# Performance work log

Hardware: AMD Instinct MI355X
Metric: run time of the kernel (lower is better)

## Reference

```python
import jax, jax.numpy as jnp
import numpy as np

# dims
R, K, N, V = 2, 3, 16384, 256          # r_len, num feat keys, nodes, raw feat dim
E, L, VE = 1, 8, 128                   # num extra keys, extra seq len, extra raw dim
LK, OUT = 1, 64                        # num label keys, out_feats (num classes)
IN, HID = 256, 512                     # in_feats, hidden
C = K + E + LK                         # num_channels for grouped conv / LayerNorm
LN_EPS = 1e-5


def _xav(key, shape, fan_in, fan_out):
    s = np.sqrt(2.0 / (fan_in + fan_out)).astype(np.float32)
    return jax.random.normal(key, shape, dtype=jnp.float32) * s


def setup_inputs() -> dict:
    key = jax.random.key(0)
    ks = jax.random.split(key, 16)
    inp = {}
    # forward args (dict-of-tensor structures flattened to stacked arrays in sorted-key order)
    inp["raw_feats"] = jax.random.normal(ks[0], (R, K, N, V), dtype=jnp.float32)
    inp["extra_feats"] = jax.random.normal(ks[1], (R, E, N, L, VE), dtype=jnp.float32)
    inp["label_feats"] = jax.random.normal(ks[2], (R, LK, N, OUT), dtype=jnp.float32)
    # per-relation embedding tables (original: uniform(-0.5,0.5); scaled for numeric tameness)
    inp["feat_emb"] = jax.random.uniform(ks[3], (R, K, V, IN), minval=-0.05, maxval=0.05, dtype=jnp.float32)
    inp["extra_emb"] = jax.random.uniform(ks[4], (R, E, VE, IN), minval=-0.05, maxval=0.05, dtype=jnp.float32)
    inp["label_emb"] = jax.random.uniform(ks[5], (R, LK, OUT, IN), minval=-0.05, maxval=0.05, dtype=jnp.float32)
    # sigmoid-attention weight vectors
    inp["w_extra"] = _xav(ks[6], (E, IN), IN, 1)      # embed_weight_r_extra
    inp["w_r"] = _xav(ks[7], (R, HID), HID, 1)        # embed_weight_r
    inp["w_global"] = _xav(ks[8], (HID,), HID, 1)     # self.w
    # grouped conv1x1 stack + LayerNorm([C,HID]) + PReLU (x2)
    inp["W1"] = _xav(ks[9], (C, IN, HID), IN, HID)
    inp["b1"] = jnp.zeros((C, HID), jnp.float32)
    inp["g1"] = jnp.ones((C, HID), jnp.float32)
    inp["be1"] = jnp.zeros((C, HID), jnp.float32)
    inp["a1"] = jnp.float32(0.25)
    inp["W2"] = _xav(ks[10], (C, HID, HID), HID, HID)
    inp["b2"] = jnp.zeros((C, HID), jnp.float32)
    inp["g2"] = jnp.ones((C, HID), jnp.float32)
    inp["be2"] = jnp.zeros((C, HID), jnp.float32)
    inp["a2"] = jnp.float32(0.25)
    # FeedForwardNet (n_layers_2 = 2)
    inp["Wf1"] = _xav(ks[11], (HID, HID), HID, HID)
    inp["bf1"] = jnp.zeros((HID,), jnp.float32)
    inp["af"] = jnp.float32(0.25)
    inp["Wf2"] = _xav(ks[12], (HID, OUT), HID, OUT)
    inp["bf2"] = jnp.zeros((OUT,), jnp.float32)
    return inp


def _prelu(x, a):
    return jnp.where(x >= 0, x, a * x)


def _ln(x, g, b):
    # LayerNorm over last two dims ([C, HID]) as in nn.LayerNorm([num_channels, hidden])
    m = jnp.mean(x, axis=(-2, -1), keepdims=True)
    v = jnp.var(x, axis=(-2, -1), keepdims=True)
    return (x - m) * jax.lax.rsqrt(v + LN_EPS) * g + b


def _attn_pool(f, w):
    # f: [N, C, D], w: [D] -> softmax(sigmoid(f @ w)) over C, weighted sum -> [N, D]
    gv = jax.nn.softmax(jax.nn.sigmoid(f @ w), axis=-1)
    return jnp.einsum('ncd,nc->nd', f, gv)


def reference(raw_feats, extra_feats, label_feats, feat_emb, extra_emb, label_emb,
              w_extra, w_r, w_global, W1, b1, g1, be1, a1, W2, b2, g2, be2, a2,
              Wf1, bf1, af, Wf2, bf2):
    outs = []
    for r in range(R):  # small fixed ensemble loop (structurally distinct params)
        mapped = jnp.einsum('knv,kvd->nkd', raw_feats[r], feat_emb[r])        # [N,K,IN]
        me = jnp.einsum('enlv,evd->enld', extra_feats[r], extra_emb[r])       # [E,N,L,IN]
        extra_out = jax.vmap(_attn_pool)(me, w_extra)                          # [E,N,IN]
        ml = jnp.einsum('knc,kcd->nkd', label_feats[r], label_emb[r])         # [N,LK,IN]
        feats = jnp.concatenate([mapped, jnp.moveaxis(extra_out, 0, 1), ml], axis=1)  # [N,C,IN]
        x = jnp.einsum('ncm,cmh->nch', feats, W1) + b1                         # grouped conv1x1
        x = _prelu(_ln(x, g1, be1), a1)
        x = jnp.einsum('nch,chk->nck', x, W2) + b2
        x = _prelu(_ln(x, g2, be2), a2)
        outs.append(_attn_pool(x, w_r[r]))                                     # [N,HID]
    h = jnp.stack(outs, axis=1)                                                # [N,R,HID]
    final = _attn_pool(h, w_global)                                            # [N,HID]
    y = _prelu(final @ Wf1 + bf1, af)
    return y @ Wf2 + bf2
```

## Files before the change

kernel.cpp:

```cpp
#include <hip/hip_runtime.h>


typedef unsigned short bf16_t;
using ushort8v = __attribute__((ext_vector_type(8))) unsigned short;
using bf16x8   = __attribute__((ext_vector_type(8))) __bf16;
using f32x4    = __attribute__((ext_vector_type(4))) float;

__device__ __forceinline__ float bf2f(bf16_t u) {
    return __uint_as_float(((unsigned int)u) << 16);
}
__device__ __forceinline__ bf16_t f2bf(float f) {
    unsigned int u = __float_as_uint(f);
    u += 0x7FFFu + ((u >> 16) & 1u);
    return (bf16_t)(u >> 16);
}
__device__ __forceinline__ float ld1(const void* p, long i, int dt) {
    return dt ? bf2f(((const bf16_t*)p)[i]) : ((const float*)p)[i];
}
__device__ __forceinline__ float4 ld4(const void* p, long i, int dt) {
    if (dt) {
        ushort4 v = *(const ushort4*)((const bf16_t*)p + i);
        return make_float4(bf2f(v.x), bf2f(v.y), bf2f(v.z), bf2f(v.w));
    }
    return *(const float4*)((const float*)p + i);
}
__device__ __forceinline__ ushort8v ld8bf(const void* p, long i, int dt) {
    if (dt) return *(const ushort8v*)((const bf16_t*)p + i);
    const float* f = (const float*)p + i;
    float4 a = *(const float4*)f, b = *(const float4*)(f + 4);
    ushort8v r;
    r[0] = f2bf(a.x); r[1] = f2bf(a.y); r[2] = f2bf(a.z); r[3] = f2bf(a.w);
    r[4] = f2bf(b.x); r[5] = f2bf(b.y); r[6] = f2bf(b.z); r[7] = f2bf(b.w);
    return r;
}
__device__ __forceinline__ float decode_scalar(const void* p, int isbf) {
    if (!isbf) return *(const float*)p;
    unsigned int u = *(const unsigned int*)p;
    if ((u & 0xFFFFu) == 0u) return __uint_as_float(u);
    return bf2f((bf16_t)(u & 0xFFFFu));
}
__device__ __forceinline__ float wave_reduce(float v) {
#pragma unroll
    for (int o = 32; o > 0; o >>= 1) v += __shfl_down(v, o, 64);
    return v;
}

__global__ void detect_k(const unsigned int* __restrict__ w, long nwords,
                         int* __restrict__ flag)
{
    const int lane = threadIdx.x;
    long idx = (long)lane * 997 + 13;
    if (idx >= nwords) idx = lane % (nwords > 0 ? nwords : 1);
    unsigned int word = w[idx];
    int e = (word >> 7) & 0xFF;
    int vote = (e >= 110 && e <= 134) ? 1 : 0;
    unsigned long long m = __ballot(vote);
    if (lane == 0) *flag = (__popcll(m) >= 32) ? 1 : 0;
}

__global__ __launch_bounds__(256) void transT_k(
    const void* __restrict__ in, long inoff, long sInZ, int Kd, int Nd,
    bf16_t* __restrict__ out, long outoff, long sOutZ,
    const int* __restrict__ flag)
{
    const int isbf = *flag;
    const long z = blockIdx.z;
    long idx = (long)blockIdx.x * 256 + threadIdx.x;
    if (idx >= (long)Kd * Nd) return;
    int k = (int)(idx / Nd), n = (int)(idx % Nd);
    out[outoff + z * sOutZ + (long)n * Kd + k] =
        f2bf(ld1(in, inoff + z * sInZ + idx, isbf));
}

__global__ __launch_bounds__(256) void fold_gemmT_k(
    const void* __restrict__ A, long aoff, long sAz, int lda,
    const void* __restrict__ B, long boff, long sBz, int ldb,
    bf16_t* __restrict__ CT, long coff, long sCz, int ldcT,
    int K, const int* __restrict__ flag)
{
    const int isbf = *flag;
    __shared__ __align__(16) float As[16][68];
    __shared__ __align__(16) float Bs[16][68];
    const int z = blockIdx.z, t = threadIdx.x;
    const int tx = t & 15, ty = t >> 4;
    const int am = t >> 2, ak = (t & 3) << 2;
    const int bn = tx << 2;
    const long aBase = aoff + z * sAz + (long)(blockIdx.y * 64 + am) * lda + ak;
    const long bBase = boff + z * sBz + (long)ty * ldb + blockIdx.x * 64 + bn;
    float acc[4][4] = {};
    for (int k0 = 0; k0 < K; k0 += 16) {
        float4 av = ld4(A, aBase + k0, isbf);
        float4 bv = ld4(B, bBase + (long)k0 * ldb, isbf);
        __syncthreads();
        As[ak + 0][am] = av.x; As[ak + 1][am] = av.y;
        As[ak + 2][am] = av.z; As[ak + 3][am] = av.w;
        *(float4*)&Bs[ty][bn] = bv;
        __syncthreads();
#pragma unroll
        for (int k = 0; k < 16; k++) {
            float4 a4 = *(const float4*)&As[k][ty << 2];
            float4 b4 = *(const float4*)&Bs[k][tx << 2];
            float ar[4] = {a4.x, a4.y, a4.z, a4.w};
            float br[4] = {b4.x, b4.y, b4.z, b4.w};
#pragma unroll
            for (int i = 0; i < 4; i++)
#pragma unroll
                for (int j = 0; j < 4; j++) acc[i][j] += ar[i] * br[j];
        }
    }
    const int cm = blockIdx.y * 64 + (ty << 2);
    const int cn = blockIdx.x * 64 + (tx << 2);
#pragma unroll
    for (int i = 0; i < 4; i++)
#pragma unroll
        for (int j = 0; j < 4; j++)
            CT[coff + z * sCz + (long)(cn + j) * ldcT + (cm + i)] = f2bf(acc[i][j]);
}

template <int BN_, int WNW_, int MODE, int CD>
__global__ __launch_bounds__(256) void mgemm(
    const void* __restrict__ A, int adt, long aoff, long sA1, long sA2, int lda,
    const bf16_t* __restrict__ BT, long boff, long sB1, long sB2,
    void* __restrict__ C, long coff, long sC1, long sC2, int ldc,
    const void* __restrict__ bias, long biasoff, long sBi1, long sBi2,
    const void* __restrict__ alpha_ptr, int K, int zdiv,
    const int* __restrict__ flag)
{
    constexpr int NJ = WNW_ / 16;
    const int isbf = *flag;
    const int adt_ = (adt == 2) ? isbf : adt;
    const int cdt = (CD == 2) ? isbf : 1;

    __shared__ __align__(16) unsigned short As[128 * 40];
    __shared__ __align__(16) unsigned short Bs[BN_ * 40];

    const int t = threadIdx.x;
    const int lane = t & 63, w = t >> 6;
    const int quad = lane >> 4, r16 = lane & 15;
    const int wy = w >> 1, wx = w & 1;
    const int z = blockIdx.z;
    const int zq = z / zdiv, zr = z % zdiv;
    const long blockM = (long)blockIdx.y * 128;
    const int  blockN = blockIdx.x * BN_;

    f32x4 acc[4][NJ];
    const f32x4 zero4 = {0.f, 0.f, 0.f, 0.f};
#pragma unroll
    for (int i = 0; i < 4; i++)
#pragma unroll
        for (int j = 0; j < NJ; j++) acc[i][j] = zero4;

    const long aBase = aoff + zq * sA1 + zr * sA2;
    const long bBase = boff + zq * sB1 + zr * sB2;

    for (int k0 = 0; k0 < K; k0 += 32) {
        ushort8v av[2], bv[BN_ / 64];
#pragma unroll
        for (int c = 0; c < 2; c++) {
            int lin = t + c * 256;
            int m = lin >> 2, kq = (lin & 3) * 8;
            av[c] = ld8bf(A, aBase + (blockM + m) * (long)lda + k0 + kq, adt_);
        }
#pragma unroll
        for (int c = 0; c < BN_ / 64; c++) {
            int lin = t + c * 256;
            int n = lin >> 2, kq = (lin & 3) * 8;
            bv[c] = *(const ushort8v*)(BT + bBase + (long)(blockN + n) * K + k0 + kq);
        }
        __syncthreads();
#pragma unroll
        for (int c = 0; c < 2; c++) {
            int lin = t + c * 256;
            int m = lin >> 2, kq = (lin & 3) * 8;
            *(ushort8v*)&As[m * 40 + kq] = av[c];
        }
#pragma unroll
        for (int c = 0; c < BN_ / 64; c++) {
            int lin = t + c * 256;
            int n = lin >> 2, kq = (lin & 3) * 8;
            *(ushort8v*)&Bs[n * 40 + kq] = bv[c];
        }
        __syncthreads();

        bf16x8 af[4], bfr[NJ];
#pragma unroll
        for (int i = 0; i < 4; i++) {
            int m = wy * 64 + i * 16 + r16;
            af[i] = __builtin_bit_cast(bf16x8, *(const ushort8v*)&As[m * 40 + quad * 8]);
        }
#pragma unroll
        for (int j = 0; j < NJ; j++) {
            int n = wx * WNW_ + j * 16 + r16;
            bfr[j] = __builtin_bit_cast(bf16x8, *(const ushort8v*)&Bs[n * 40 + quad * 8]);
        }
#pragma unroll
        for (int i = 0; i < 4; i++)
#pragma unroll
            for (int j = 0; j < NJ; j++)
                acc[i][j] = __builtin_amdgcn_mfma_f32_16x16x32_bf16(
                    af[i], bfr[j], acc[i][j], 0, 0, 0);
    }

    const float alpha = (MODE == 2) ? decode_scalar(alpha_ptr, isbf) : 0.f;
    const long cBase = coff + zq * sC1 + zr * sC2;
#pragma unroll
    for (int j = 0; j < NJ; j++) {
        const int n = blockN + wx * WNW_ + j * 16 + r16;
        const float bz = (MODE >= 1)
            ? ld1(bias, biasoff + zq * sBi1 + zr * sBi2 + n, isbf) : 0.f;
#pragma unroll
        for (int i = 0; i < 4; i++) {
            const long m0 = blockM + wy * 64 + i * 16 + quad * 4;
#pragma unroll
            for (int rg = 0; rg < 4; rg++) {
                float v = acc[i][j][rg] + bz;
                if (MODE == 2) v = (v >= 0.f) ? v : alpha * v;
                const long off = cBase + (m0 + rg) * (long)ldc + n;
                if (cdt) ((bf16_t*)C)[off] = f2bf(v);
                else     ((float*)C)[off] = v;
            }
        }
    }
}

__global__ __launch_bounds__(256) void pool_extra_k(
    const bf16_t* __restrict__ ME, long sMEz, const void* __restrict__ wx,
    float* __restrict__ EO, long sEOz, const int* __restrict__ flag)
{
    const int isbf = *flag;
    const int n = blockIdx.x, t = threadIdx.x;
    const bf16_t* base = ME + blockIdx.y * sMEz + (long)n * 2048;
    float v[8];
#pragma unroll
    for (int l = 0; l < 8; l++) v[l] = bf2f(base[l * 256 + t]);
    const float w = ld1(wx, t, isbf);
    __shared__ float red[8][4];
    const int lane = t & 63, wid = t >> 6;
#pragma unroll
    for (int l = 0; l < 8; l++) {
        float pr = wave_reduce(v[l] * w);
        if (lane == 0) red[l][wid] = pr;
    }
    __syncthreads();
    float gv[8], ssum = 0.f;
#pragma unroll
    for (int l = 0; l < 8; l++) {
        float sc = red[l][0] + red[l][1] + red[l][2] + red[l][3];
        float sg = 1.f / (1.f + expf(-sc));
        float e = expf(sg);
        gv[l] = e; ssum += e;
    }
    const float inv = 1.f / ssum;
    float o = 0.f;
#pragma unroll
    for (int l = 0; l < 8; l++) o += gv[l] * inv * v[l];
    EO[blockIdx.y * sEOz + (long)n * 256 + t] = o;
}

__global__ __launch_bounds__(256) void ln1_k(
    bf16_t* __restrict__ X, const void* __restrict__ g,
    const void* __restrict__ be, const void* __restrict__ alpha_ptr,
    const int* __restrict__ flag)
{
    const int isbf = *flag;
    const int n = blockIdx.x, t = threadIdx.x;
    bf16_t* row = X + (long)n * 2560;
    float v[10], s = 0.f, sq = 0.f;
#pragma unroll
    for (int i = 0; i < 10; i++) {
        float x = bf2f(row[i * 256 + t]);
        v[i] = x; s += x; sq += x * x;
    }
    __shared__ float redS[4], redQ[4];
    const int lane = t & 63, wid = t >> 6;
    float ws_ = wave_reduce(s), wq = wave_reduce(sq);
    if (lane == 0) { redS[wid] = ws_; redQ[wid] = wq; }
    __syncthreads();
    const float S = redS[0] + redS[1] + redS[2] + redS[3];
    const float Q = redQ[0] + redQ[1] + redQ[2] + redQ[3];
    const float mean = S * (1.f / 2560.f);
    const float rstd = rsqrtf(fmaxf(Q * (1.f / 2560.f) - mean * mean, 0.f) + 1e-5f);
    const float alpha = decode_scalar(alpha_ptr, isbf);
#pragma unroll
    for (int i = 0; i < 10; i++) {
        int e = i * 256 + t;
        float y = (v[i] - mean) * rstd * ld1(g, e, isbf) + ld1(be, e, isbf);
        row[e] = f2bf((y >= 0.f) ? y : alpha * y);
    }
}

__global__ __launch_bounds__(256) void ln2_pool_k(
    const bf16_t* __restrict__ X, long sXz, const void* __restrict__ g,
    const void* __restrict__ be, const void* __restrict__ alpha_ptr,
    const void* __restrict__ wr,
    bf16_t* __restrict__ H, const int* __restrict__ flag)
{
    const int isbf = *flag;
    const int n = blockIdx.x, t = threadIdx.x, rr = blockIdx.y;
    const bf16_t* row = X + rr * sXz + (long)n * 2560;
    float v[5][2], s = 0.f, sq = 0.f;
#pragma unroll
    for (int c = 0; c < 5; c++)
#pragma unroll
        for (int hi = 0; hi < 2; hi++) {
            float x = bf2f(row[c * 512 + hi * 256 + t]);
            v[c][hi] = x; s += x; sq += x * x;
        }
    __shared__ float redS[4], redQ[4];
    const int lane = t & 63, wid = t >> 6;
    float ws_ = wave_reduce(s), wq = wave_reduce(sq);
    if (lane == 0) { redS[wid] = ws_; redQ[wid] = wq; }
    __syncthreads();
    const float S = redS[0] + redS[1] + redS[2] + redS[3];
    const float Q = redQ[0] + redQ[1] + redQ[2] + redQ[3];
    const float mean = S * (1.f / 2560.f);
    const float rstd = rsqrtf(fmaxf(Q * (1.f / 2560.f) - mean * mean, 0.f) + 1e-5f);
    const float alpha = decode_scalar(alpha_ptr, isbf);
    const float w0 = ld1(wr, (long)rr * 512 + t, isbf);
    const float w1 = ld1(wr, (long)rr * 512 + t + 256, isbf);
    float p[5];
#pragma unroll
    for (int c = 0; c < 5; c++) {
        p[c] = 0.f;
#pragma unroll
        for (int hi = 0; hi < 2; hi++) {
            int e = c * 512 + hi * 256 + t;
            float y = (v[c][hi] - mean) * rstd * ld1(g, e, isbf) + ld1(be, e, isbf);
            y = (y >= 0.f) ? y : alpha * y;
            v[c][hi] = y;
            p[c] += y * (hi ? w1 : w0);
        }
    }
    __shared__ float redP[5][4];
#pragma unroll
    for (int c = 0; c < 5; c++) {
        float pr = wave_reduce(p[c]);
        if (lane == 0) redP[c][wid] = pr;
    }
    __syncthreads();
    float gv[5], ssum = 0.f;
#pragma unroll
    for (int c = 0; c < 5; c++) {
        float sc = redP[c][0] + redP[c][1] + redP[c][2] + redP[c][3];
        float sg = 1.f / (1.f + expf(-sc));
        float e = expf(sg);
        gv[c] = e; ssum += e;
    }
    const float inv = 1.f / ssum;
#pragma unroll
    for (int hi = 0; hi < 2; hi++) {
        float o = 0.f;
#pragma unroll
        for (int c = 0; c < 5; c++) o += gv[c] * inv * v[c][hi];
        H[(long)n * 1024 + rr * 512 + hi * 256 + t] = f2bf(o);
    }
}

__global__ __launch_bounds__(256) void gpool_k(
    const bf16_t* __restrict__ H, const void* __restrict__ wg,
    bf16_t* __restrict__ F, const int* __restrict__ flag)
{
    const int isbf = *flag;
    const int n = blockIdx.x, t = threadIdx.x;
    const bf16_t* base = H + (long)n * 1024;
    const float w0 = ld1(wg, t, isbf), w1 = ld1(wg, t + 256, isbf);
    float v[2][2], p[2];
#pragma unroll
    for (int r = 0; r < 2; r++) {
        v[r][0] = bf2f(base[r * 512 + t]);
        v[r][1] = bf2f(base[r * 512 + 256 + t]);
        p[r] = v[r][0] * w0 + v[r][1] * w1;
    }
    __shared__ float red[2][4];
    const int lane = t & 63, wid = t >> 6;
#pragma unroll
    for (int r = 0; r < 2; r++) {
        float pr = wave_reduce(p[r]);
        if (lane == 0) red[r][wid] = pr;
    }
    __syncthreads();
    float gv[2], ssum = 0.f;
#pragma unroll
    for (int r = 0; r < 2; r++) {
        float sc = red[r][0] + red[r][1] + red[r][2] + red[r][3];
        float sg = 1.f / (1.f + expf(-sc));
        float e = expf(sg);
        gv[r] = e; ssum += e;
    }
    const float inv = 1.f / ssum;
#pragma unroll
    for (int hi = 0; hi < 2; hi++) {
        F[(long)n * 512 + hi * 256 + t] =
            f2bf((gv[0] * v[0][hi] + gv[1] * v[1][hi]) * inv);
    }
}

extern "C" void kernel_launch(void* const* d_in, const int* in_sizes, int n_in,
                              void* d_out, int out_size, void* d_ws, size_t ws_size,
                              hipStream_t stream)
{
    const void* raw   = d_in[0];
    const void* extra = d_in[1];
    const void* lbl   = d_in[2];
    const void* femb  = d_in[3];
    const void* eemb  = d_in[4];
    const void* lemb  = d_in[5];
    const void* wx    = d_in[6];
    const void* wr    = d_in[7];
    const void* wg    = d_in[8];
    const void* W1    = d_in[9];
    const void* b1    = d_in[10];
    const void* g1    = d_in[11];
    const void* be1   = d_in[12];
    const void* a1    = d_in[13];
    const void* W2    = d_in[14];
    const void* b2    = d_in[15];
    const void* g2    = d_in[16];
    const void* be2   = d_in[17];
    const void* a2    = d_in[18];
    const void* Wf1   = d_in[19];
    const void* bf1   = d_in[20];
    const void* af    = d_in[21];
    const void* Wf2   = d_in[22];
    const void* bf2b  = d_in[23];

    int*    flag  = (int*)d_ws;
    bf16_t* MfT   = (bf16_t*)((char*)d_ws + 256);
    bf16_t* MlT   = MfT + 786432;
    bf16_t* W1c3T = MlT + 65536;
    bf16_t* W2T   = W1c3T + 131072;
    bf16_t* Wf1T  = W2T + 1310720;
    bf16_t* Wf2T  = Wf1T + 262144;
    bf16_t* eT    = Wf2T + 32768;
    char*   arena = (char*)(eT + 65536);
    const size_t fixedBytes = 256 + 2654208 * 2;

    int Nc = 16384;
    while (Nc > 128 && fixedBytes + (size_t)Nc * 24576 > ws_size) Nc >>= 1;
    const int NCH = 16384 / Nc;

    bf16_t* x1  = (bf16_t*)arena;
    bf16_t* x2  = (bf16_t*)(arena + (size_t)Nc * 10240);
    float*  eo  = (float*) (arena + (size_t)Nc * 20480);
    bf16_t* hbc = (bf16_t*)(arena + (size_t)Nc * 22528);
    bf16_t* mec = x1;
    bf16_t* fin = x2;
    bf16_t* zb  = x2 + (size_t)Nc * 512;

    dim3 blk(256);

    detect_k<<<1, 64, 0, stream>>>((const unsigned int*)raw,
                                   (long)in_sizes[0] / 2, flag);

    transT_k<<<dim3(1024, 1, 5), blk, 0, stream>>>(W2, 0, 262144, 512, 512,
                                                   W2T, 0, 262144, flag);
    transT_k<<<dim3(512, 1, 1), blk, 0, stream>>>(W1, 3L * 131072, 0, 256, 512,
                                                  W1c3T, 0, 0, flag);
    transT_k<<<dim3(1024, 1, 1), blk, 0, stream>>>(Wf1, 0, 0, 512, 512,
                                                   Wf1T, 0, 0, flag);
    transT_k<<<dim3(128, 1, 1), blk, 0, stream>>>(Wf2, 0, 0, 512, 64,
                                                  Wf2T, 0, 0, flag);
    transT_k<<<dim3(128, 1, 2), blk, 0, stream>>>(eemb, 0, 32768, 128, 256,
                                                  eT, 0, 32768, flag);

    for (int r = 0; r < 2; r++) {
        fold_gemmT_k<<<dim3(8, 4, 3), blk, 0, stream>>>(
            femb, (long)r * 196608, 65536, 256,
            W1, 0, 131072, 512,
            MfT, (long)r * 393216, 131072, 256, 256, flag);
    }
    fold_gemmT_k<<<dim3(8, 1, 2), blk, 0, stream>>>(
        lemb, 0, 16384, 256,
        W1, 4L * 131072, 0, 512,
        MlT, 0, 32768, 64, 256, flag);

    for (int c = 0; c < NCH; c++) {
        const long n0 = (long)c * Nc;

        mgemm<128, 64, 0, 1><<<dim3(2, Nc * 8 / 128, 2), blk, 0, stream>>>(
            extra, 2, n0 * 1024, 16777216, 0, 128,
            eT, 0, 32768, 0,
            mec, 0, (long)Nc * 8 * 256, 0, 256,
            nullptr, 0, 0, 0, nullptr, 128, 1, flag);
        pool_extra_k<<<dim3(Nc, 2), blk, 0, stream>>>(
            mec, (long)Nc * 8 * 256, wx, eo, (long)Nc * 256, flag);

        mgemm<128, 64, 1, 1><<<dim3(4, Nc / 128, 6), blk, 0, stream>>>(
            raw, 2, n0 * 256, 12582912, 4194304, 256,
            MfT, 0, 393216, 131072,
            x1, 0, (long)Nc * 2560, 512, 2560,
            b1, 0, 0, 512, nullptr, 256, 3, flag);
        mgemm<128, 64, 1, 1><<<dim3(4, Nc / 128, 2), blk, 0, stream>>>(
            eo, 0, 0, (long)Nc * 256, 0, 256,
            W1c3T, 0, 0, 0,
            x1, 3L * 512, (long)Nc * 2560, 0, 2560,
            b1, 3L * 512, 0, 0, nullptr, 256, 1, flag);
        mgemm<128, 64, 1, 1><<<dim3(4, Nc / 128, 2), blk, 0, stream>>>(
            lbl, 2, n0 * 64, 1048576, 0, 64,
            MlT, 0, 32768, 0,
            x1, 4L * 512, (long)Nc * 2560, 0, 2560,
            b1, 4L * 512, 0, 0, nullptr, 64, 1, flag);

        ln1_k<<<2 * Nc, blk, 0, stream>>>(x1, g1, be1, a1, flag);

        mgemm<128, 64, 1, 1><<<dim3(4, Nc / 128, 10), blk, 0, stream>>>(
            x1, 1, 0, (long)Nc * 2560, 512, 2560,
            W2T, 0, 0, 262144,
            x2, 0, (long)Nc * 2560, 512, 2560,
            b2, 0, 0, 512, nullptr, 512, 5, flag);

        ln2_pool_k<<<dim3(Nc, 2), blk, 0, stream>>>(
            x2, (long)Nc * 2560, g2, be2, a2, wr, hbc, flag);

        gpool_k<<<Nc, blk, 0, stream>>>(hbc, wg, fin, flag);

        mgemm<128, 64, 2, 1><<<dim3(4, Nc / 128, 1), blk, 0, stream>>>(
            fin, 1, 0, 0, 0, 512,
            Wf1T, 0, 0, 0,
            zb, 0, 0, 0, 512,
            bf1, 0, 0, 0, af, 512, 1, flag);
        mgemm<64, 32, 1, 2><<<dim3(1, Nc / 128, 1), blk, 0, stream>>>(
            zb, 1, 0, 0, 0, 512,
            Wf2T, 0, 0, 0,
            d_out, n0 * 64, 0, 0, 64,
            bf2b, 0, 0, 0, nullptr, 512, 1, flag);
    }
}
```

Measured before the change: 1.064 ms.

## Use direct global-to-LDS loads in GEMM and fuse pooling and LayerNorm kernels

The GEMM staging path now uses global_load_lds to copy bf16 tiles straight into unpadded LDS, replacing the register round-trip. The extra-feature GEMM and its sigmoid attention pool are fused into one kernel that writes a bf16 pooled output, so the 8x intermediate never goes to memory. LN2, the per-relation pool and the global pool are merged into one kernel that accumulates into LDS with shared atomics, and LN1 switches to 320-thread blocks with 8-wide vector loads. Dropping the LDS padding may add bank conflicts on the fragment reads, and the LDS atomics and bf16 rounding of the extra output change numerics slightly.

Result: slower. 1.355 ms (+27.4%).

```diff
diff --git a/kernel.cpp b/kernel.cpp
--- a/kernel.cpp
+++ b/kernel.cpp
@@ -1,4 +1,5 @@
 #include <hip/hip_runtime.h>
+#include <stdint.h>
 
 
 typedef unsigned short bf16_t;
@@ -43,6 +44,12 @@
 #pragma unroll
     for (int o = 32; o > 0; o >>= 1) v += __shfl_down(v, o, 64);
     return v;
+}
+__device__ __forceinline__ void gl2lds16(const void* g, void* l) {
+    using gptr_t = const __attribute__((address_space(1))) unsigned int*;
+    using lptr_t = __attribute__((address_space(3))) unsigned int*;
+    __builtin_amdgcn_global_load_lds((gptr_t)(uintptr_t)g, (lptr_t)(uintptr_t)l,
+                                     16, 0, 0);
 }
 
 __global__ void detect_k(const unsigned int* __restrict__ w, long nwords,
@@ -131,13 +138,15 @@
     const int adt_ = (adt == 2) ? isbf : adt;
     const int cdt = (CD == 2) ? isbf : 1;
 
-    __shared__ __align__(16) unsigned short As[128 * 40];
-    __shared__ __align__(16) unsigned short Bs[BN_ * 40];
+    __shared__ __align__(16) bf16_t As[128 * 32];
+    __shared__ __align__(16) bf16_t Bs[BN_ * 32];
 
     const int t = threadIdx.x;
-    const int lane = t & 63, w = t >> 6;
+    const int lane = t & 63, wv = t >> 6;
     const int quad = lane >> 4, r16 = lane & 15;
-    const int wy = w >> 1, wx = w & 1;
+    const int wy = wv >> 1, wxx = wv & 1;
+    const int srow = lane >> 2;
+    const int scol = (lane & 3) * 8;
     const int z = blockIdx.z;
     const int zq = z / zdiv, zr = z % zdiv;
     const long blockM = (long)blockIdx.y * 128;
@@ -154,45 +163,42 @@
     const long bBase = boff + zq * sB1 + zr * sB2;
 
     for (int k0 = 0; k0 < K; k0 += 32) {
-        ushort8v av[2], bv[BN_ / 64];
-#pragma unroll
-        for (int c = 0; c < 2; c++) {
-            int lin = t + c * 256;
-            int m = lin >> 2, kq = (lin & 3) * 8;
-            av[c] = ld8bf(A, aBase + (blockM + m) * (long)lda + k0 + kq, adt_);
-        }
-#pragma unroll
-        for (int c = 0; c < BN_ / 64; c++) {
-            int lin = t + c * 256;
-            int n = lin >> 2, kq = (lin & 3) * 8;
-            bv[c] = *(const ushort8v*)(BT + bBase + (long)(blockN + n) * K + k0 + kq);
-        }
-        __syncthreads();
-#pragma unroll
-        for (int c = 0; c < 2; c++) {
-            int lin = t + c * 256;
-            int m = lin >> 2, kq = (lin & 3) * 8;
-            *(ushort8v*)&As[m * 40 + kq] = av[c];
-        }
-#pragma unroll
-        for (int c = 0; c < BN_ / 64; c++) {
-            int lin = t + c * 256;
-            int n = lin >> 2, kq = (lin & 3) * 8;
-            *(ushort8v*)&Bs[n * 40 + kq] = bv[c];
+        __syncthreads();
+        if (adt_) {
+#pragma unroll
+            for (int s = 0; s < 2; s++) {
+                int rbase = wv * 32 + s * 16;
+                const bf16_t* g = (const bf16_t*)A + aBase
+                    + (blockM + rbase + srow) * (long)lda + k0 + scol;
+                gl2lds16(g, &As[rbase * 32]);
+            }
+        } else {
+#pragma unroll
+            for (int c = 0; c < 2; c++) {
+                int lin = t + c * 256;
+                int m = lin >> 2, kq = (lin & 3) * 8;
+                ushort8v v = ld8bf(A, aBase + (blockM + m) * (long)lda + k0 + kq, 0);
+                *(ushort8v*)&As[m * 32 + kq] = v;
+            }
+        }
+#pragma unroll
+        for (int s = 0; s < BN_ / 64; s++) {
+            int rbase = wv * (BN_ / 4) + s * 16;
+            const bf16_t* g = BT + bBase
+                + (long)(blockN + rbase + srow) * K + k0 + scol;
+            gl2lds16(g, &Bs[rbase * 32]);
         }
         __syncthreads();
 
         bf16x8 af[4], bfr[NJ];
 #pragma unroll
-        for (int i = 0; i < 4; i++) {
-            int m = wy * 64 + i * 16 + r16;
-            af[i] = __builtin_bit_cast(bf16x8, *(const ushort8v*)&As[m * 40 + quad * 8]);
-        }
-#pragma unroll
-        for (int j = 0; j < NJ; j++) {
-            int n = wx * WNW_ + j * 16 + r16;
-            bfr[j] = __builtin_bit_cast(bf16x8, *(const ushort8v*)&Bs[n * 40 + quad * 8]);
-        }
+        for (int i = 0; i < 4; i++)
+            af[i] = __builtin_bit_cast(bf16x8,
+                *(const ushort8v*)&As[(wy * 64 + i * 16 + r16) * 32 + quad * 8]);
+#pragma unroll
+        for (int j = 0; j < NJ; j++)
+            bfr[j] = __builtin_bit_cast(bf16x8,
+                *(const ushort8v*)&Bs[(wxx * WNW_ + j * 16 + r16) * 32 + quad * 8]);
 #pragma unroll
         for (int i = 0; i < 4; i++)
 #pragma unroll
@@ -205,7 +211,7 @@
     const long cBase = coff + zq * sC1 + zr * sC2;
 #pragma unroll
     for (int j = 0; j < NJ; j++) {
-        const int n = blockN + wx * WNW_ + j * 16 + r16;
+        const int n = blockN + wxx * WNW_ + j * 16 + r16;
         const float bz = (MODE >= 1)
             ? ld1(bias, biasoff + zq * sBi1 + zr * sBi2 + n, isbf) : 0.f;
 #pragma unroll
@@ -223,41 +229,151 @@
     }
 }
 
-__global__ __launch_bounds__(256) void pool_extra_k(
-    const bf16_t* __restrict__ ME, long sMEz, const void* __restrict__ wx,
-    float* __restrict__ EO, long sEOz, const int* __restrict__ flag)
+__global__ __launch_bounds__(256) void megemm_pool(
+    const void* __restrict__ A, long aoff, long sAr,
+    const bf16_t* __restrict__ BT, long sBr,
+    const void* __restrict__ wx,
+    bf16_t* __restrict__ EO, long sEOr,
+    const int* __restrict__ flag)
 {
     const int isbf = *flag;
-    const int n = blockIdx.x, t = threadIdx.x;
-    const bf16_t* base = ME + blockIdx.y * sMEz + (long)n * 2048;
-    float v[8];
-#pragma unroll
-    for (int l = 0; l < 8; l++) v[l] = bf2f(base[l * 256 + t]);
-    const float w = ld1(wx, t, isbf);
-    __shared__ float red[8][4];
-    const int lane = t & 63, wid = t >> 6;
-#pragma unroll
-    for (int l = 0; l < 8; l++) {
-        float pr = wave_reduce(v[l] * w);
-        if (lane == 0) red[l][wid] = pr;
+    __shared__ __align__(16) bf16_t As[128 * 32];
+    __shared__ __align__(16) bf16_t Bs[256 * 32];
+    __shared__ float sred[128][2];
+    __shared__ float gvs[128];
+
+    const int t = threadIdx.x;
+    const int lane = t & 63, wv = t >> 6;
+    const int quad = lane >> 4, r16 = lane & 15;
+    const int wy = wv >> 1, wxx = wv & 1;
+    const int srow = lane >> 2, scol = (lane & 3) * 8;
+    const int r = blockIdx.z;
+    const long blockM = (long)blockIdx.y * 128;
+
+    f32x4 acc[4][8];
+    const f32x4 zero4 = {0.f, 0.f, 0.f, 0.f};
+#pragma unroll
+    for (int i = 0; i < 4; i++)
+#pragma unroll
+        for (int j = 0; j < 8; j++) acc[i][j] = zero4;
+
+    const long aBase = aoff + (long)r * sAr;
+    const long bBase = (long)r * sBr;
+
+    for (int k0 = 0; k0 < 128; k0 += 32) {
+        __syncthreads();
+        if (isbf) {
+#pragma unroll
+            for (int s = 0; s < 2; s++) {
+                int rbase = wv * 32 + s * 16;
+                const bf16_t* g = (const bf16_t*)A + aBase
+                    + (blockM + rbase + srow) * 128L + k0 + scol;
+                gl2lds16(g, &As[rbase * 32]);
+            }
+        } else {
+#pragma unroll
+            for (int c = 0; c < 2; c++) {
+                int lin = t + c * 256;
+                int m = lin >> 2, kq = (lin & 3) * 8;
+                ushort8v v = ld8bf(A, aBase + (blockM + m) * 128L + k0 + kq, 0);
+                *(ushort8v*)&As[m * 32 + kq] = v;
+            }
+        }
+#pragma unroll
+        for (int s = 0; s < 4; s++) {
+            int rbase = wv * 64 + s * 16;
+            const bf16_t* g = BT + bBase + (long)(rbase + srow) * 128 + k0 + scol;
+            gl2lds16(g, &Bs[rbase * 32]);
+        }
+        __syncthreads();
+
+        bf16x8 af[4], bfr[8];
+#pragma unroll
+        for (int i = 0; i < 4; i++)
+            af[i] = __builtin_bit_cast(bf16x8,
+                *(const ushort8v*)&As[(wy * 64 + i * 16 + r16) * 32 + quad * 8]);
+#pragma unroll
+        for (int j = 0; j < 8; j++)
+            bfr[j] = __builtin_bit_cast(bf16x8,
+                *(const ushort8v*)&Bs[(wxx * 128 + j * 16 + r16) * 32 + quad * 8]);
+#pragma unroll
+        for (int i = 0; i < 4; i++)
+#pragma unroll
+            for (int j = 0; j < 8; j++)
+                acc[i][j] = __builtin_amdgcn_mfma_f32_16x16x32_bf16(
+                    af[i], bfr[j], acc[i][j], 0, 0, 0);
+    }
+
+    float wxv[8];
+#pragma unroll
+    for (int j = 0; j < 8; j++)
+        wxv[j] = ld1(wx, wxx * 128 + j * 16 + r16, isbf);
+
+    float pp[4][4];
+#pragma unroll
+    for (int i = 0; i < 4; i++)
+#pragma unroll
+        for (int rg = 0; rg < 4; rg++) {
+            float s = 0.f;
+#pragma unroll
+            for (int j = 0; j < 8; j++) s += acc[i][j][rg] * wxv[j];
+            pp[i][rg] = s;
+        }
+#pragma unroll
+    for (int o = 1; o < 16; o <<= 1)
+#pragma unroll
+        for (int i = 0; i < 4; i++)
+#pragma unroll
+            for (int rg = 0; rg < 4; rg++)
+                pp[i][rg] += __shfl_xor(pp[i][rg], o, 64);
+    if (r16 == 0) {
+#pragma unroll
+        for (int i = 0; i < 4; i++)
+#pragma unroll
+            for (int rg = 0; rg < 4; rg++)
+                sred[wy * 64 + i * 16 + quad * 4 + rg][wxx] = pp[i][rg];
     }
     __syncthreads();
-    float gv[8], ssum = 0.f;
-#pragma unroll
-    for (int l = 0; l < 8; l++) {
-        float sc = red[l][0] + red[l][1] + red[l][2] + red[l][3];
-        float sg = 1.f / (1.f + expf(-sc));
-        float e = expf(sg);
-        gv[l] = e; ssum += e;
-    }
-    const float inv = 1.f / ssum;
-    float o = 0.f;
-#pragma unroll
-    for (int l = 0; l < 8; l++) o += gv[l] * inv * v[l];
-    EO[blockIdx.y * sEOz + (long)n * 256 + t] = o;
-}
-
-__global__ __launch_bounds__(256) void ln1_k(
+    if (t < 16) {
+        float e[8], sm = 0.f;
+#pragma unroll
+        for (int l = 0; l < 8; l++) {
+            float sc = sred[t * 8 + l][0] + sred[t * 8 + l][1];
+            float sg = 1.f / (1.f + expf(-sc));
+            e[l] = expf(sg); sm += e[l];
+        }
+        float inv = 1.f / sm;
+#pragma unroll
+        for (int l = 0; l < 8; l++) gvs[t * 8 + l] = e[l] * inv;
+    }
+    __syncthreads();
+
+    float gvl[4][4];
+#pragma unroll
+    for (int i = 0; i < 4; i++)
+#pragma unroll
+        for (int rg = 0; rg < 4; rg++)
+            gvl[i][rg] = gvs[wy * 64 + i * 16 + quad * 4 + rg];
+
+#pragma unroll
+    for (int i = 0; i < 4; i++) {
+        const long nodeBase = (blockM + wy * 64 + i * 16) >> 3;
+        const int myNode = (int)nodeBase + (quad >> 1);
+#pragma unroll
+        for (int j = 0; j < 8; j++) {
+            float s = 0.f;
+#pragma unroll
+            for (int rg = 0; rg < 4; rg++) s += acc[i][j][rg] * gvl[i][rg];
+            s += __shfl_xor(s, 16, 64);
+            if ((quad & 1) == 0) {
+                int col = wxx * 128 + j * 16 + r16;
+                EO[(long)r * sEOr + (long)myNode * 256 + col] = f2bf(s);
+            }
+        }
+    }
+}
+
+__global__ __launch_bounds__(320) void ln1_k(
     bf16_t* __restrict__ X, const void* __restrict__ g,
     const void* __restrict__ be, const void* __restrict__ alpha_ptr,
     const int* __restrict__ flag)
@@ -265,134 +381,116 @@
     const int isbf = *flag;
     const int n = blockIdx.x, t = threadIdx.x;
     bf16_t* row = X + (long)n * 2560;
-    float v[10], s = 0.f, sq = 0.f;
-#pragma unroll
-    for (int i = 0; i < 10; i++) {
-        float x = bf2f(row[i * 256 + t]);
-        v[i] = x; s += x; sq += x * x;
-    }
-    __shared__ float redS[4], redQ[4];
+    const int e0 = t * 8;
+    ushort8v xv = *(const ushort8v*)&row[e0];
+    float v[8], s = 0.f, sq = 0.f;
+#pragma unroll
+    for (int k = 0; k < 8; k++) {
+        float x = bf2f(xv[k]);
+        v[k] = x; s += x; sq += x * x;
+    }
+    __shared__ float redS[5], redQ[5];
     const int lane = t & 63, wid = t >> 6;
     float ws_ = wave_reduce(s), wq = wave_reduce(sq);
     if (lane == 0) { redS[wid] = ws_; redQ[wid] = wq; }
     __syncthreads();
-    const float S = redS[0] + redS[1] + redS[2] + redS[3];
-    const float Q = redQ[0] + redQ[1] + redQ[2] + redQ[3];
+    float S = 0.f, Q = 0.f;
+#pragma unroll
+    for (int i = 0; i < 5; i++) { S += redS[i]; Q += redQ[i]; }
     const float mean = S * (1.f / 2560.f);
     const float rstd = rsqrtf(fmaxf(Q * (1.f / 2560.f) - mean * mean, 0.f) + 1e-5f);
     const float alpha = decode_scalar(alpha_ptr, isbf);
-#pragma unroll
-    for (int i = 0; i < 10; i++) {
-        int e = i * 256 + t;
-        float y = (v[i] - mean) * rstd * ld1(g, e, isbf) + ld1(be, e, isbf);
-        row[e] = f2bf((y >= 0.f) ? y : alpha * y);
-    }
-}
-
-__global__ __launch_bounds__(256) void ln2_pool_k(
-    const bf16_t* __restrict__ X, long sXz, const void* __restrict__ g,
+    ushort8v gv8 = ld8bf(g, e0, isbf), bv8 = ld8bf(be, e0, isbf);
+    ushort8v ov;
+#pragma unroll
+    for (int k = 0; k < 8; k++) {
+        float y = (v[k] - mean) * rstd * bf2f(gv8[k]) + bf2f(bv8[k]);
+        ov[k] = f2bf((y >= 0.f) ? y : alpha * y);
+    }
+    *(ushort8v*)&row[e0] = ov;
+}
+
+__global__ __launch_bounds__(320) void ln2_gpool_k(
+    const bf16_t* __restrict__ X, long sXr, const void* __restrict__ g,
     const void* __restrict__ be, const void* __restrict__ alpha_ptr,
-    const void* __restrict__ wr,
-    bf16_t* __restrict__ H, const int* __restrict__ flag)
-{
-    const int isbf = *flag;
-    const int n = blockIdx.x, t = threadIdx.x, rr = blockIdx.y;
-    const bf16_t* row = X + rr * sXz + (long)n * 2560;
-    float v[5][2], s = 0.f, sq = 0.f;
-#pragma unroll
-    for (int c = 0; c < 5; c++)
-#pragma unroll
-        for (int hi = 0; hi < 2; hi++) {
-            float x = bf2f(row[c * 512 + hi * 256 + t]);
-            v[c][hi] = x; s += x; sq += x * x;
-        }
-    __shared__ float redS[4], redQ[4];
-    const int lane = t & 63, wid = t >> 6;
-    float ws_ = wave_reduce(s), wq = wave_reduce(sq);
-    if (lane == 0) { redS[wid] = ws_; redQ[wid] = wq; }
-    __syncthreads();
-    const float S = redS[0] + redS[1] + redS[2] + redS[3];
-    const float Q = redQ[0] + redQ[1] + redQ[2] + redQ[3];
-    const float mean = S * (1.f / 2560.f);
-    const float rstd = rsqrtf(fmaxf(Q * (1.f / 2560.f) - mean * mean, 0.f) + 1e-5f);
-    const float alpha = decode_scalar(alpha_ptr, isbf);
-    const float w0 = ld1(wr, (long)rr * 512 + t, isbf);
-    const float w1 = ld1(wr, (long)rr * 512 + t + 256, isbf);
-    float p[5];
-#pragma unroll
-    for (int c = 0; c < 5; c++) {
-        p[c] = 0.f;
-#pragma unroll
-        for (int hi = 0; hi < 2; hi++) {
-            int e = c * 512 + hi * 256 + t;
-            float y = (v[c][hi] - mean) * rstd * ld1(g, e, isbf) + ld1(be, e, isbf);
-            y = (y >= 0.f) ? y : alpha * y;
-            v[c][hi] = y;
-            p[c] += y * (hi ? w1 : w0);
-        }
-    }
-    __shared__ float redP[5][4];
-#pragma unroll
-    for (int c = 0; c < 5; c++) {
-        float pr = wave_reduce(p[c]);
-        if (lane == 0) redP[c][wid] = pr;
-    }
-    __syncthreads();
-    float gv[5], ssum = 0.f;
-#pragma unroll
-    for (int c = 0; c < 5; c++) {
-        float sc = redP[c][0] + redP[c][1] + redP[c][2] + redP[c][3];
-        float sg = 1.f / (1.f + expf(-sc));
-        float e = expf(sg);
-        gv[c] = e; ssum += e;
-    }
-    const float inv = 1.f / ssum;
-#pragma unroll
-    for (int hi = 0; hi < 2; hi++) {
-        float o = 0.f;
-#pragma unroll
-        for (int c = 0; c < 5; c++) o += gv[c] * inv * v[c][hi];
-        H[(long)n * 1024 + rr * 512 + hi * 256 + t] = f2bf(o);
-    }
-}
-
-__global__ __launch_bounds__(256) void gpool_k(
-    const bf16_t* __restrict__ H, const void* __restrict__ wg,
+    const void* __restrict__ wr, const void* __restrict__ wg,
     bf16_t* __restrict__ F, const int* __restrict__ flag)
 {
     const int isbf = *flag;
     const int n = blockIdx.x, t = threadIdx.x;
-    const bf16_t* base = H + (long)n * 1024;
-    const float w0 = ld1(wg, t, isbf), w1 = ld1(wg, t + 256, isbf);
-    float v[2][2], p[2];
-#pragma unroll
+    const int lane = t & 63, wid = t >> 6;
+    const int e0 = t * 8;
+
+    __shared__ float hacc[2][512];
+    __shared__ float redS[2][5], redQ[2][5], redP[2][5], redG[2][5];
+    for (int i = t; i < 1024; i += 320) ((float*)hacc)[i] = 0.f;
+
+    const float alpha = decode_scalar(alpha_ptr, isbf);
+    ushort8v gv8 = ld8bf(g, e0, isbf), bv8 = ld8bf(be, e0, isbf);
+
     for (int r = 0; r < 2; r++) {
-        v[r][0] = bf2f(base[r * 512 + t]);
-        v[r][1] = bf2f(base[r * 512 + 256 + t]);
-        p[r] = v[r][0] * w0 + v[r][1] * w1;
-    }
-    __shared__ float red[2][4];
-    const int lane = t & 63, wid = t >> 6;
+        const bf16_t* row = X + (long)r * sXr + (long)n * 2560;
+        ushort8v xv = *(const ushort8v*)&row[e0];
+        float v[8], s = 0.f, sq = 0.f;
+#pragma unroll
+        for (int k = 0; k < 8; k++) {
+            float x = bf2f(xv[k]);
+            v[k] = x; s += x; sq += x * x;
+        }
+        float ws_ = wave_reduce(s), wq = wave_reduce(sq);
+        if (lane == 0) { redS[r][wid] = ws_; redQ[r][wid] = wq; }
+        __syncthreads();
+        float S = 0.f, Q = 0.f;
+#pragma unroll
+        for (int i = 0; i < 5; i++) { S += redS[r][i]; Q += redQ[r][i]; }
+        const float mean = S * (1.f / 2560.f);
+        const float rstd = rsqrtf(fmaxf(Q * (1.f / 2560.f) - mean * mean, 0.f) + 1e-5f);
+        float pc = 0.f;
+#pragma unroll
+        for (int k = 0; k < 8; k++) {
+            float y = (v[k] - mean) * rstd * bf2f(gv8[k]) + bf2f(bv8[k]);
+            y = (y >= 0.f) ? y : alpha * y;
+            v[k] = y;
+            pc += y * ld1(wr, (long)r * 512 + ((e0 + k) & 511), isbf);
+        }
+        float wp = wave_reduce(pc);
+        if (lane == 0) redP[r][wid] = wp;
+        __syncthreads();
+        float ssum = 0.f, eown = 0.f;
+#pragma unroll
+        for (int c = 0; c < 5; c++) {
+            float sg = 1.f / (1.f + expf(-redP[r][c]));
+            float e = expf(sg);
+            if (c == wid) eown = e;
+            ssum += e;
+        }
+        const float gvc = eown / ssum;
+#pragma unroll
+        for (int k = 0; k < 8; k++)
+            atomicAdd(&hacc[r][(e0 + k) & 511], v[k] * gvc);
+        __syncthreads();
+    }
+
+    float pr[2] = {0.f, 0.f};
+    for (int h = t; h < 512; h += 320) {
+        float w = ld1(wg, h, isbf);
+        pr[0] += hacc[0][h] * w;
+        pr[1] += hacc[1][h] * w;
+    }
 #pragma unroll
     for (int r = 0; r < 2; r++) {
-        float pr = wave_reduce(p[r]);
-        if (lane == 0) red[r][wid] = pr;
+        float wp = wave_reduce(pr[r]);
+        if (lane == 0) redG[r][wid] = wp;
     }
     __syncthreads();
-    float gv[2], ssum = 0.f;
-#pragma unroll
-    for (int r = 0; r < 2; r++) {
-        float sc = red[r][0] + red[r][1] + red[r][2] + red[r][3];
-        float sg = 1.f / (1.f + expf(-sc));
-        float e = expf(sg);
-        gv[r] = e; ssum += e;
-    }
-    const float inv = 1.f / ssum;
-#pragma unroll
-    for (int hi = 0; hi < 2; hi++) {
-        F[(long)n * 512 + hi * 256 + t] =
-            f2bf((gv[0] * v[0][hi] + gv[1] * v[1][hi]) * inv);
-    }
+    float sc0 = 0.f, sc1 = 0.f;
+#pragma unroll
+    for (int i = 0; i < 5; i++) { sc0 += redG[0][i]; sc1 += redG[1][i]; }
+    float eg0 = expf(1.f / (1.f + expf(-sc0)));
+    float eg1 = expf(1.f / (1.f + expf(-sc1)));
+    float inv = 1.f / (eg0 + eg1);
+    for (int h = t; h < 512; h += 320)
+        F[(long)n * 512 + h] = f2bf((eg0 * hacc[0][h] + eg1 * hacc[1][h]) * inv);
 }
 
 extern "C" void kernel_launch(void* const* d_in, const int* in_sizes, int n_in,
@@ -436,18 +534,16 @@
     const size_t fixedBytes = 256 + 2654208 * 2;
 
     int Nc = 16384;
-    while (Nc > 128 && fixedBytes + (size_t)Nc * 24576 > ws_size) Nc >>= 1;
+    while (Nc > 128 && fixedBytes + (size_t)Nc * 21504 > ws_size) Nc >>= 1;
     const int NCH = 16384 / Nc;
 
-    bf16_t* x1  = (bf16_t*)arena;
-    bf16_t* x2  = (bf16_t*)(arena + (size_t)Nc * 10240);
-    float*  eo  = (float*) (arena + (size_t)Nc * 20480);
-    bf16_t* hbc = (bf16_t*)(arena + (size_t)Nc * 22528);
-    bf16_t* mec = x1;
-    bf16_t* fin = x2;
-    bf16_t* zb  = x2 + (size_t)Nc * 512;
-
-    dim3 blk(256);
+    bf16_t* x1 = (bf16_t*)arena;
+    bf16_t* x2 = (bf16_t*)(arena + (size_t)Nc * 10240);
+    bf16_t* eo = (bf16_t*)(arena + (size_t)Nc * 20480);
+    bf16_t* fin = x1;
+    bf16_t* zb  = x1 + (size_t)Nc * 512;
+
+    dim3 blk(256), blk5(320);
 
     detect_k<<<1, 64, 0, stream>>>((const unsigned int*)raw,
                                    (long)in_sizes[0] / 2, flag);
@@ -477,13 +573,9 @@
     for (int c = 0; c < NCH; c++) {
         const long n0 = (long)c * Nc;
 
-        mgemm<128, 64, 0, 1><<<dim3(2, Nc * 8 / 128, 2), blk, 0, stream>>>(
-            extra, 2, n0 * 1024, 16777216, 0, 128,
-            eT, 0, 32768, 0,
-            mec, 0, (long)Nc * 8 * 256, 0, 256,
-            nullptr, 0, 0, 0, nullptr, 128, 1, flag);
-        pool_extra_k<<<dim3(Nc, 2), blk, 0, stream>>>(
-            mec, (long)Nc * 8 * 256, wx, eo, (long)Nc * 256, flag);
+        megemm_pool<<<dim3(1, Nc / 16, 2), blk, 0, stream>>>(
+            extra, n0 * 1024, 16777216,
+            eT, 32768, wx, eo, (long)Nc * 256, flag);
 
         mgemm<128, 64, 1, 1><<<dim3(4, Nc / 128, 6), blk, 0, stream>>>(
             raw, 2, n0 * 256, 12582912, 4194304, 256,
@@ -491,7 +583,7 @@
             x1, 0, (long)Nc * 2560, 512, 2560,
             b1, 0, 0, 512, nullptr, 256, 3, flag);
         mgemm<128, 64, 1, 1><<<dim3(4, Nc / 128, 2), blk, 0, stream>>>(
-            eo, 0, 0, (long)Nc * 256, 0, 256,
+            eo, 1, 0, (long)Nc * 256, 0, 256,
             W1c3T, 0, 0, 0,
             x1, 3L * 512, (long)Nc * 2560, 0, 2560,
             b1, 3L * 512, 0, 0, nullptr, 256, 1, flag);
@@ -501,7 +593,7 @@
             x1, 4L * 512, (long)Nc * 2560, 0, 2560,
             b1, 4L * 512, 0, 0, nullptr, 64, 1, flag);
 
-        ln1_k<<<2 * Nc, blk, 0, stream>>>(x1, g1, be1, a1, flag);
+        ln1_k<<<2 * Nc, blk5, 0, stream>>>(x1, g1, be1, a1, flag);
 
         mgemm<128, 64, 1, 1><<<dim3(4, Nc / 128, 10), blk, 0, stream>>>(
             x1, 1, 0, (long)Nc * 2560, 512, 2560,
@@ -509,10 +601,8 @@
             x2, 0, (long)Nc * 2560, 512, 2560,
             b2, 0, 0, 512, nullptr, 512, 5, flag);
 
-        ln2_pool_k<<<dim3(Nc, 2), blk, 0, stream>>>(
-            x2, (long)Nc * 2560, g2, be2, a2, wr, hbc, flag);
-
-        gpool_k<<<Nc, blk, 0, stream>>>(hbc, wg, fin, flag);
+        ln2_gpool_k<<<Nc, blk5, 0, stream>>>(
+            x2, (long)Nc * 2560, g2, be2, a2, wr, wg, fin, flag);
 
         mgemm<128, 64, 2, 1><<<dim3(4, Nc / 128, 1), blk, 0, stream>>>(
             fin, 1, 0, 0, 0, 512,
```
